# Kernel tuning notes

Hardware: AMD Instinct MI355X
Metric: run time of the kernel (lower is better)

## Reference

```python
import jax, jax.numpy as jnp
import numpy as np

B, SIDES, L = 8192, 2, 64   # batch, (left,right) trees, leaves per tree (complete binary tree)
V, D, C, R = 10000, 128, 128, 7  # vocab, word_dim, cpr_dim, num_rels


def setup_inputs() -> dict:
    key = jax.random.key(0)
    ks = jax.random.split(key, 9)
    s = 0.05
    return {
        "tokens": jax.random.randint(ks[0], (B, SIDES, L), 0, V, dtype=jnp.int32),
        "voc_w": jax.random.normal(ks[1], (V, D), dtype=jnp.float32) * s,
        "voc_b": jax.random.normal(ks[2], (D,), dtype=jnp.float32) * s,
        "cps_w": jax.random.normal(ks[3], (D, 2 * D), dtype=jnp.float32) * s,
        "cps_b": jax.random.normal(ks[4], (D,), dtype=jnp.float32) * s,
        "cpr_w": jax.random.normal(ks[5], (C, 2 * D), dtype=jnp.float32) * s,
        "cpr_b": jax.random.normal(ks[6], (C,), dtype=jnp.float32) * s,
        "sm_w": jax.random.normal(ks[7], (R, C), dtype=jnp.float32) * s,
        "sm_b": jax.random.normal(ks[8], (R,), dtype=jnp.float32) * s,
    }


def reference(tokens, voc_w, voc_b, cps_w, cps_b, cpr_w, cpr_b, sm_w, sm_b):
    # Leaf composition: one-hot @ Linear(voc_size, word_dim) == embedding gather + bias
    h = voc_w[tokens] + voc_b  # [B, 2, L, D]
    # Level-by-level composition of complete binary trees: cat(left,right) -> cps -> tanh
    n = h.shape[2]
    while n > 1:
        h = h.reshape(h.shape[0], SIDES, n // 2, 2 * h.shape[-1])  # adjacent pairs -> concat
        h = jnp.tanh(jnp.einsum('bsnk,dk->bsnd', h, cps_w) + cps_b)
        n //= 2
    root = h.reshape(h.shape[0], -1)  # [B, 2*D]: cat(left_cps, right_cps)
    z = jax.nn.leaky_relu(root @ cpr_w.T + cpr_b)  # LeakyReLU default slope 0.01
    return jax.nn.softmax(z @ sm_w.T + sm_b, axis=-1)  # [B, R]
```

## Files before the change

kernel.cpp:

```cpp
#include <hip/hip_runtime.h>
#include <hip/hip_bf16.h>


typedef __attribute__((ext_vector_type(8))) short bf16x8;
typedef __attribute__((ext_vector_type(4))) float f32x4;

#define VOCN (10000 * 128)
#define CPSN (128 * 256)
#define CPRN (128 * 256)

__device__ __forceinline__ uint pk2(float a, float b) {
  union { __hip_bfloat162 h2; uint u; } cv;
  cv.h2 = __float22bfloat162_rn(make_float2(a, b));
  return cv.u;
}
__device__ __forceinline__ float2 up2(uint u) {
  union { uint u; __hip_bfloat162 h2; } cv; cv.u = u;
  return __bfloat1622float2(cv.h2);
}
__device__ __forceinline__ float fast_tanh(float x) {
  const float t = x * x;
  float u = __builtin_fmaf(t, -0.05396825397f, 0.13333333333f);
  u = __builtin_fmaf(t, u, -0.33333333333f);
  u = __builtin_fmaf(t, u, 1.0f);
  return x * u;
}
__device__ __forceinline__ int sf(int r) { return r ^ ((r >> 3) & 7); }

__global__ void prep_kernel(const float* __restrict__ voc_w, const float* __restrict__ voc_b,
                            const float* __restrict__ cps_w, const float* __restrict__ cpr_w,
                            ushort* __restrict__ ws) {
  const int i4 = (blockIdx.x * 256 + threadIdx.x) * 4;
  if (i4 >= VOCN + CPSN + CPRN) return;
  float4 v;
  if (i4 < VOCN) {
    v = *(const float4*)(voc_w + i4);
    const float4 bb = *(const float4*)(voc_b + (i4 & 127));
    v.x += bb.x; v.y += bb.y; v.z += bb.z; v.w += bb.w;
  } else if (i4 < VOCN + CPSN) {
    v = *(const float4*)(cps_w + (i4 - VOCN));
  } else {
    v = *(const float4*)(cpr_w + (i4 - VOCN - CPSN));
  }
  uint2 w; w.x = pk2(v.x, v.y); w.y = pk2(v.z, v.w);
  *(uint2*)(ws + i4) = w;
}

#define MFMA16(Ax, Bx, Cx) __builtin_amdgcn_mfma_f32_16x16x32_bf16(Ax, Bx, Cx, 0, 0, 0)

template<int TOFF>
__device__ __forceinline__ void tile16(const char* hb, const bf16x8 (&A)[2][8],
                                       int RL, int RR, f32x4& aA, f32x4& aB) {
  bf16x8 bl[4], br[4];
#pragma unroll
  for (int q = 0; q < 4; ++q) {
    bl[q] = *(const bf16x8*)(hb + RL + TOFF + q * 4096);
    br[q] = *(const bf16x8*)(hb + RR + TOFF + q * 4096);
  }
#pragma unroll
  for (int q = 0; q < 4; ++q) {
    aA = MFMA16(A[0][q], bl[q], aA);
    aB = MFMA16(A[1][q], bl[q], aB);
  }
#pragma unroll
  for (int q = 0; q < 4; ++q) {
    aA = MFMA16(A[0][4 + q], br[q], aA);
    aB = MFMA16(A[1][4 + q], br[q], aB);
  }
}

template<int TOFF>
__device__ __forceinline__ void wtile(char* hb, int W, const f32x4& aA, const f32x4& aB) {
  uint2 w0, w1;
  w0.x = pk2(fast_tanh(aA[0]), fast_tanh(aA[1]));
  w0.y = pk2(fast_tanh(aA[2]), fast_tanh(aA[3]));
  w1.x = pk2(fast_tanh(aB[0]), fast_tanh(aB[1]));
  w1.y = pk2(fast_tanh(aB[2]), fast_tanh(aB[3]));
  *(uint2*)(hb + W + TOFF) = w0;
  *(uint2*)(hb + W + TOFF + 2048) = w1;
}

template<int PRE>
__global__ __launch_bounds__(256, 4)
void trnn_kernel(const int* __restrict__ tokens,
                 const float* __restrict__ voc_w, const float* __restrict__ voc_b,
                 const float* __restrict__ cps_w, const float* __restrict__ cps_b,
                 const float* __restrict__ cpr_w, const float* __restrict__ cpr_b,
                 const float* __restrict__ sm_w, const float* __restrict__ sm_b,
                 const ushort* __restrict__ wsb, float* __restrict__ out) {
  __shared__ ushort h[16384];
  const int tid = threadIdx.x;
  const int lane = tid & 63, wv = tid >> 6;
  const int l15 = lane & 15, lh = lane >> 4;
  const int b = blockIdx.x;
  char* hb = (char*)h;

  const ushort* voc_bf = wsb;
  const ushort* cps_bf = wsb + VOCN;
  const ushort* cpr_bf = wsb + VOCN + CPSN;

  const int lhb = lh * 1024;
  const int RLa = lhb + sf(2 * l15) * 16;
  const int RRa = lhb + sf(2 * l15 + 1) * 16;
  const int RLb = lhb + sf(2 * l15 + 32) * 16;
  const int RRb = lhb + sf(2 * l15 + 33) * 16;
  const int RL3 = (((l15 >> 3) & 1) << 14) + lhb + sf((l15 & 7) * 2) * 16;
  const int RR3 = (((l15 >> 3) & 1) << 14) + lhb + sf((l15 & 7) * 2 + 1) * 16;
  const int RL4 = (((l15 >> 2) & 1) << 14) + lhb + sf((l15 & 3) * 2) * 16;
  const int RR4 = (((l15 >> 2) & 1) << 14) + lhb + sf((l15 & 3) * 2 + 1) * 16;
  const int RL5 = (((l15 >> 1) & 1) << 14) + lhb + sf((l15 & 1) * 2) * 16;
  const int RR5 = (((l15 >> 1) & 1) << 14) + lhb + sf((l15 & 1) * 2 + 1) * 16;
  const int RL6 = ((l15 & 1) << 14) + lhb;
  const int RR6 = ((l15 & 1) << 14) + lhb + 16;
  const int dpart = (((wv * 32 + lh * 4) >> 3) << 10) + ((lh & 1) << 3);
  const int Wa = sf(l15) * 16 + dpart;
  const int Wb = sf(l15 + 16) * 16 + dpart;
  const int W3 = (((l15 >> 3) & 1) << 14) + sf(l15 & 7) * 16 + dpart;
  const int W4 = (((l15 >> 2) & 1) << 14) + sf(l15 & 3) * 16 + dpart;
  const int W5 = (((l15 >> 1) & 1) << 14) + sf(l15 & 1) * 16 + dpart;
  const int W6 = ((l15 & 1) << 14) + dpart;

  bf16x8 A[2][8];
  f32x4 bias[2];
#pragma unroll
  for (int mt = 0; mt < 2; ++mt) {
    const int d = wv * 32 + mt * 16 + l15;
#pragma unroll
    for (int kt = 0; kt < 8; ++kt) {
      const int k = kt * 32 + lh * 8;
      if constexpr (PRE) {
        A[mt][kt] = *(const bf16x8*)(cps_bf + d * 256 + k);
      } else {
        const float* p = cps_w + d * 256 + k;
        float4 lo = *(const float4*)p, hi = *(const float4*)(p + 4);
        union { bf16x8 v; uint4 u; } f;
        f.u.x = pk2(lo.x, lo.y); f.u.y = pk2(lo.z, lo.w);
        f.u.z = pk2(hi.x, hi.y); f.u.w = pk2(hi.z, hi.w);
        A[mt][kt] = f.v;
      }
    }
    const float4 bb = *(const float4*)(cps_b + wv * 32 + mt * 16 + lh * 4);
    bias[mt][0] = bb.x; bias[mt][1] = bb.y; bias[mt][2] = bb.z; bias[mt][3] = bb.w;
  }

  {
    const int tree = tid >> 7, lf = (tid >> 1) & 63, half = tid & 1;
    const int tok = tokens[b * 128 + tree * 64 + lf];
    char* tp = hb + tree * 16384 + half * 8192 + sf(lf) * 16;
    if constexpr (PRE) {
      const ushort* vr = voc_bf + tok * 128 + half * 64;
#pragma unroll
      for (int j = 0; j < 8; ++j)
        *(uint4*)(tp + j * 1024) = *(const uint4*)(vr + j * 8);
    } else {
      const float* vw = voc_w + tok * 128 + half * 64;
      const float* vb = voc_b + half * 64;
#pragma unroll
      for (int j = 0; j < 8; ++j) {
        float4 v0 = *(const float4*)(vw + j * 8);
        float4 v1 = *(const float4*)(vw + j * 8 + 4);
        float4 q0 = *(const float4*)(vb + j * 8);
        float4 q1 = *(const float4*)(vb + j * 8 + 4);
        uint4 w;
        w.x = pk2(v0.x + q0.x, v0.y + q0.y);
        w.y = pk2(v0.z + q0.z, v0.w + q0.w);
        w.z = pk2(v1.x + q1.x, v1.y + q1.y);
        w.w = pk2(v1.z + q1.z, v1.w + q1.w);
        *(uint4*)(tp + j * 1024) = w;
      }
    }
  }
  __syncthreads();

  {
    f32x4 a0 = bias[0], b0 = bias[1], a1 = bias[0], b1 = bias[1];
    f32x4 a2 = bias[0], b2 = bias[1], a3 = bias[0], b3 = bias[1];
    tile16<0>(hb, A, RLa, RRa, a0, b0);
    tile16<0>(hb, A, RLb, RRb, a1, b1);
    tile16<16384>(hb, A, RLa, RRa, a2, b2);
    tile16<16384>(hb, A, RLb, RRb, a3, b3);
    __syncthreads();
    wtile<0>(hb, Wa, a0, b0);
    wtile<0>(hb, Wb, a1, b1);
    wtile<16384>(hb, Wa, a2, b2);
    wtile<16384>(hb, Wb, a3, b3);
    __syncthreads();
  }
  {
    f32x4 a0 = bias[0], b0 = bias[1], a1 = bias[0], b1 = bias[1];
    tile16<0>(hb, A, RLa, RRa, a0, b0);
    tile16<16384>(hb, A, RLa, RRa, a1, b1);
    __syncthreads();
    wtile<0>(hb, Wa, a0, b0);
    wtile<16384>(hb, Wa, a1, b1);
    __syncthreads();
  }
  {
    f32x4 a0 = bias[0], b0 = bias[1];
    tile16<0>(hb, A, RL3, RR3, a0, b0);
    __syncthreads();
    wtile<0>(hb, W3, a0, b0);
    __syncthreads();
  }
  {
    f32x4 a0 = bias[0], b0 = bias[1];
    tile16<0>(hb, A, RL4, RR4, a0, b0);
    __syncthreads();
    if (l15 < 8) wtile<0>(hb, W4, a0, b0);
    __syncthreads();
  }
  {
    f32x4 a0 = bias[0], b0 = bias[1];
    tile16<0>(hb, A, RL5, RR5, a0, b0);
    __syncthreads();
    if (l15 < 4) wtile<0>(hb, W5, a0, b0);
    __syncthreads();
  }
  {
    f32x4 a0 = bias[0], b0 = bias[1];
    tile16<0>(hb, A, RL6, RR6, a0, b0);
    __syncthreads();
    if (l15 < 2) wtile<0>(hb, W6, a0, b0);
    __syncthreads();
  }


  {
    const int half = tid >> 7, c = tid & 127;
    const char* rp = hb + half * 16384;
    float acc = 0.f;
#pragma unroll 4
    for (int ch = 0; ch < 16; ++ch) {
      uint4 u = *(const uint4*)(rp + ch * 1024);
      float2 e0 = up2(u.x), e1 = up2(u.y), e2 = up2(u.z), e3 = up2(u.w);
      if constexpr (PRE) {
        uint4 wq = *(const uint4*)(cpr_bf + c * 256 + half * 128 + ch * 8);
        float2 w0 = up2(wq.x), w1 = up2(wq.y), w2 = up2(wq.z), w3 = up2(wq.w);
        acc += e0.x * w0.x + e0.y * w0.y + e1.x * w1.x + e1.y * w1.y
             + e2.x * w2.x + e2.y * w2.y + e3.x * w3.x + e3.y * w3.y;
      } else {
        const float* wr = cpr_w + c * 256 + half * 128 + ch * 8;
        float4 w0 = *(const float4*)wr, w1 = *(const float4*)(wr + 4);
        acc += e0.x * w0.x + e0.y * w0.y + e1.x * w0.z + e1.y * w0.w
             + e2.x * w1.x + e2.y * w1.y + e3.x * w1.z + e3.y * w1.w;
      }
    }
    *(float*)(hb + ((tid >> 4) << 10) + 512 + ((tid & 15) << 2)) = acc;
  }
  __syncthreads();
  if (tid < 128) {
    const float p0 = *(const float*)(hb + ((tid >> 4) << 10) + 512 + ((tid & 15) << 2));
    const int j1 = tid + 128;
    const float p1 = *(const float*)(hb + ((j1 >> 4) << 10) + 512 + ((j1 & 15) << 2));
    float z = p0 + p1 + cpr_b[tid];
    z = z > 0.f ? z : 0.01f * z;
    *(float*)(hb + 16384 + ((tid >> 3) << 10) + 768 + ((tid & 7) << 2)) = z;
  }
  __syncthreads();

  if (wv == 0) {
    const int i0 = lane, i1 = 64 + lane;
    const float za = *(const float*)(hb + 16384 + ((i0 >> 3) << 10) + 768 + ((i0 & 7) << 2));
    const float zc = *(const float*)(hb + 16384 + ((i1 >> 3) << 10) + 768 + ((i1 & 7) << 2));
    float p[7];
#pragma unroll
    for (int j = 0; j < 7; ++j)
      p[j] = za * sm_w[j * 128 + lane] + zc * sm_w[j * 128 + 64 + lane];
#pragma unroll
    for (int j = 0; j < 7; ++j) {
      float v = p[j];
#pragma unroll
      for (int off = 32; off >= 1; off >>= 1) v += __shfl_xor(v, off, 64);
      p[j] = v + sm_b[j];
    }
    float mx = p[0];
#pragma unroll
    for (int j = 1; j < 7; ++j) mx = fmaxf(mx, p[j]);
    float e[7], s = 0.f;
#pragma unroll
    for (int j = 0; j < 7; ++j) { e[j] = __expf(p[j] - mx); s += e[j]; }
    const float inv = 1.f / s;
    if (lane == 0) {
#pragma unroll
      for (int j = 0; j < 7; ++j) out[b * 7 + j] = e[j] * inv;
    }
  }
}

extern "C" void kernel_launch(void* const* d_in, const int* in_sizes, int n_in,
                              void* d_out, int out_size, void* d_ws, size_t ws_size,
                              hipStream_t stream) {
  const int*   tokens = (const int*)  d_in[0];
  const float* voc_w  = (const float*)d_in[1];
  const float* voc_b  = (const float*)d_in[2];
  const float* cps_w  = (const float*)d_in[3];
  const float* cps_b  = (const float*)d_in[4];
  const float* cpr_w  = (const float*)d_in[5];
  const float* cpr_b  = (const float*)d_in[6];
  const float* sm_w   = (const float*)d_in[7];
  const float* sm_b   = (const float*)d_in[8];
  float* out = (float*)d_out;

  const int B = in_sizes[0] / 128;
  const size_t need = (size_t)(VOCN + CPSN + CPRN) * sizeof(ushort);

  if (ws_size >= need) {
    ushort* ws = (ushort*)d_ws;
    const int tot4 = (VOCN + CPSN + CPRN) / 4;
    prep_kernel<<<(tot4 + 255) / 256, 256, 0, stream>>>(voc_w, voc_b, cps_w, cpr_w, ws);
    trnn_kernel<1><<<B, 256, 0, stream>>>(tokens, voc_w, voc_b, cps_w, cps_b,
                                          cpr_w, cpr_b, sm_w, sm_b, ws, out);
  } else {
    trnn_kernel<0><<<B, 256, 0, stream>>>(tokens, voc_w, voc_b, cps_w, cps_b,
                                          cpr_w, cpr_b, sm_w, sm_b,
                                          (const ushort*)d_ws, out);
  }
}
```

Baseline: 166.8 us.

## Use 512-thread blocks with one wave group per tree side

Doubles the block to 512 threads. Waves 4-7 handle the right tree and waves 0-3 the left, so each wave does half the MFMA tiles per level. The leaf gather and the cpr reduction are split four ways, and the partial sums are combined in shared memory. The aim is more waves in flight to hide LDS and MFMA latency. In exchange, every wave now loads its own copy of the cps A-fragments into registers, and occupancy limits from the register budget may change under launch_bounds(512,4).

```diff
diff --git a/kernel.cpp b/kernel.cpp
--- a/kernel.cpp
+++ b/kernel.cpp
@@ -48,14 +48,13 @@
 
 #define MFMA16(Ax, Bx, Cx) __builtin_amdgcn_mfma_f32_16x16x32_bf16(Ax, Bx, Cx, 0, 0, 0)
 
-template<int TOFF>
 __device__ __forceinline__ void tile16(const char* hb, const bf16x8 (&A)[2][8],
                                        int RL, int RR, f32x4& aA, f32x4& aB) {
   bf16x8 bl[4], br[4];
 #pragma unroll
   for (int q = 0; q < 4; ++q) {
-    bl[q] = *(const bf16x8*)(hb + RL + TOFF + q * 4096);
-    br[q] = *(const bf16x8*)(hb + RR + TOFF + q * 4096);
+    bl[q] = *(const bf16x8*)(hb + RL + q * 4096);
+    br[q] = *(const bf16x8*)(hb + RR + q * 4096);
   }
 #pragma unroll
   for (int q = 0; q < 4; ++q) {
@@ -69,19 +68,18 @@
   }
 }
 
-template<int TOFF>
 __device__ __forceinline__ void wtile(char* hb, int W, const f32x4& aA, const f32x4& aB) {
   uint2 w0, w1;
   w0.x = pk2(fast_tanh(aA[0]), fast_tanh(aA[1]));
   w0.y = pk2(fast_tanh(aA[2]), fast_tanh(aA[3]));
   w1.x = pk2(fast_tanh(aB[0]), fast_tanh(aB[1]));
   w1.y = pk2(fast_tanh(aB[2]), fast_tanh(aB[3]));
-  *(uint2*)(hb + W + TOFF) = w0;
-  *(uint2*)(hb + W + TOFF + 2048) = w1;
+  *(uint2*)(hb + W) = w0;
+  *(uint2*)(hb + W + 2048) = w1;
 }
 
 template<int PRE>
-__global__ __launch_bounds__(256, 4)
+__global__ __launch_bounds__(512, 4)
 void trnn_kernel(const int* __restrict__ tokens,
                  const float* __restrict__ voc_w, const float* __restrict__ voc_b,
                  const float* __restrict__ cps_w, const float* __restrict__ cps_b,
@@ -92,6 +90,8 @@
   const int tid = threadIdx.x;
   const int lane = tid & 63, wv = tid >> 6;
   const int l15 = lane & 15, lh = lane >> 4;
+  const int wq = wv & 3;
+  const int toff = (wv >> 2) << 14;
   const int b = blockIdx.x;
   char* hb = (char*)h;
 
@@ -99,32 +99,32 @@
   const ushort* cps_bf = wsb + VOCN;
   const ushort* cpr_bf = wsb + VOCN + CPSN;
 
-  const int lhb = lh * 1024;
+  const int lhb = toff + lh * 1024;
   const int RLa = lhb + sf(2 * l15) * 16;
   const int RRa = lhb + sf(2 * l15 + 1) * 16;
   const int RLb = lhb + sf(2 * l15 + 32) * 16;
   const int RRb = lhb + sf(2 * l15 + 33) * 16;
-  const int RL3 = (((l15 >> 3) & 1) << 14) + lhb + sf((l15 & 7) * 2) * 16;
-  const int RR3 = (((l15 >> 3) & 1) << 14) + lhb + sf((l15 & 7) * 2 + 1) * 16;
-  const int RL4 = (((l15 >> 2) & 1) << 14) + lhb + sf((l15 & 3) * 2) * 16;
-  const int RR4 = (((l15 >> 2) & 1) << 14) + lhb + sf((l15 & 3) * 2 + 1) * 16;
-  const int RL5 = (((l15 >> 1) & 1) << 14) + lhb + sf((l15 & 1) * 2) * 16;
-  const int RR5 = (((l15 >> 1) & 1) << 14) + lhb + sf((l15 & 1) * 2 + 1) * 16;
-  const int RL6 = ((l15 & 1) << 14) + lhb;
-  const int RR6 = ((l15 & 1) << 14) + lhb + 16;
-  const int dpart = (((wv * 32 + lh * 4) >> 3) << 10) + ((lh & 1) << 3);
+  const int RL3 = lhb + sf((l15 & 7) * 2) * 16;
+  const int RR3 = lhb + sf((l15 & 7) * 2 + 1) * 16;
+  const int RL4 = lhb + sf((l15 & 3) * 2) * 16;
+  const int RR4 = lhb + sf((l15 & 3) * 2 + 1) * 16;
+  const int RL5 = lhb + sf((l15 & 1) * 2) * 16;
+  const int RR5 = lhb + sf((l15 & 1) * 2 + 1) * 16;
+  const int RL6 = lhb;
+  const int RR6 = lhb + 16;
+  const int dpart = toff + (((wq * 32 + lh * 4) >> 3) << 10) + ((lh & 1) << 3);
   const int Wa = sf(l15) * 16 + dpart;
   const int Wb = sf(l15 + 16) * 16 + dpart;
-  const int W3 = (((l15 >> 3) & 1) << 14) + sf(l15 & 7) * 16 + dpart;
-  const int W4 = (((l15 >> 2) & 1) << 14) + sf(l15 & 3) * 16 + dpart;
-  const int W5 = (((l15 >> 1) & 1) << 14) + sf(l15 & 1) * 16 + dpart;
-  const int W6 = ((l15 & 1) << 14) + dpart;
+  const int W3 = sf(l15 & 7) * 16 + dpart;
+  const int W4 = sf(l15 & 3) * 16 + dpart;
+  const int W5 = sf(l15 & 1) * 16 + dpart;
+  const int W6 = dpart;
 
   bf16x8 A[2][8];
   f32x4 bias[2];
 #pragma unroll
   for (int mt = 0; mt < 2; ++mt) {
-    const int d = wv * 32 + mt * 16 + l15;
+    const int d = wq * 32 + mt * 16 + l15;
 #pragma unroll
     for (int kt = 0; kt < 8; ++kt) {
       const int k = kt * 32 + lh * 8;
@@ -139,24 +139,24 @@
         A[mt][kt] = f.v;
       }
     }
-    const float4 bb = *(const float4*)(cps_b + wv * 32 + mt * 16 + lh * 4);
+    const float4 bb = *(const float4*)(cps_b + wq * 32 + mt * 16 + lh * 4);
     bias[mt][0] = bb.x; bias[mt][1] = bb.y; bias[mt][2] = bb.z; bias[mt][3] = bb.w;
   }
 
   {
-    const int tree = tid >> 7, lf = (tid >> 1) & 63, half = tid & 1;
+    const int tree = tid >> 8, lf = (tid >> 2) & 63, qr = tid & 3;
     const int tok = tokens[b * 128 + tree * 64 + lf];
-    char* tp = hb + tree * 16384 + half * 8192 + sf(lf) * 16;
+    char* tp = hb + tree * 16384 + qr * 4096 + sf(lf) * 16;
     if constexpr (PRE) {
-      const ushort* vr = voc_bf + tok * 128 + half * 64;
-#pragma unroll
-      for (int j = 0; j < 8; ++j)
+      const ushort* vr = voc_bf + tok * 128 + qr * 32;
+#pragma unroll
+      for (int j = 0; j < 4; ++j)
         *(uint4*)(tp + j * 1024) = *(const uint4*)(vr + j * 8);
     } else {
-      const float* vw = voc_w + tok * 128 + half * 64;
-      const float* vb = voc_b + half * 64;
-#pragma unroll
-      for (int j = 0; j < 8; ++j) {
+      const float* vw = voc_w + tok * 128 + qr * 32;
+      const float* vb = voc_b + qr * 32;
+#pragma unroll
+      for (int j = 0; j < 4; ++j) {
         float4 v0 = *(const float4*)(vw + j * 8);
         float4 v1 = *(const float4*)(vw + j * 8 + 4);
         float4 q0 = *(const float4*)(vb + j * 8);
@@ -174,85 +174,77 @@
 
   {
     f32x4 a0 = bias[0], b0 = bias[1], a1 = bias[0], b1 = bias[1];
-    f32x4 a2 = bias[0], b2 = bias[1], a3 = bias[0], b3 = bias[1];
-    tile16<0>(hb, A, RLa, RRa, a0, b0);
-    tile16<0>(hb, A, RLb, RRb, a1, b1);
-    tile16<16384>(hb, A, RLa, RRa, a2, b2);
-    tile16<16384>(hb, A, RLb, RRb, a3, b3);
-    __syncthreads();
-    wtile<0>(hb, Wa, a0, b0);
-    wtile<0>(hb, Wb, a1, b1);
-    wtile<16384>(hb, Wa, a2, b2);
-    wtile<16384>(hb, Wb, a3, b3);
-    __syncthreads();
-  }
-  {
-    f32x4 a0 = bias[0], b0 = bias[1], a1 = bias[0], b1 = bias[1];
-    tile16<0>(hb, A, RLa, RRa, a0, b0);
-    tile16<16384>(hb, A, RLa, RRa, a1, b1);
-    __syncthreads();
-    wtile<0>(hb, Wa, a0, b0);
-    wtile<16384>(hb, Wa, a1, b1);
-    __syncthreads();
-  }
-  {
-    f32x4 a0 = bias[0], b0 = bias[1];
-    tile16<0>(hb, A, RL3, RR3, a0, b0);
-    __syncthreads();
-    wtile<0>(hb, W3, a0, b0);
-    __syncthreads();
-  }
-  {
-    f32x4 a0 = bias[0], b0 = bias[1];
-    tile16<0>(hb, A, RL4, RR4, a0, b0);
-    __syncthreads();
-    if (l15 < 8) wtile<0>(hb, W4, a0, b0);
-    __syncthreads();
-  }
-  {
-    f32x4 a0 = bias[0], b0 = bias[1];
-    tile16<0>(hb, A, RL5, RR5, a0, b0);
-    __syncthreads();
-    if (l15 < 4) wtile<0>(hb, W5, a0, b0);
-    __syncthreads();
-  }
-  {
-    f32x4 a0 = bias[0], b0 = bias[1];
-    tile16<0>(hb, A, RL6, RR6, a0, b0);
-    __syncthreads();
-    if (l15 < 2) wtile<0>(hb, W6, a0, b0);
-    __syncthreads();
-  }
-
-
-  {
-    const int half = tid >> 7, c = tid & 127;
-    const char* rp = hb + half * 16384;
+    tile16(hb, A, RLa, RRa, a0, b0);
+    tile16(hb, A, RLb, RRb, a1, b1);
+    __syncthreads();
+    wtile(hb, Wa, a0, b0);
+    wtile(hb, Wb, a1, b1);
+    __syncthreads();
+  }
+  {
+    f32x4 a0 = bias[0], b0 = bias[1];
+    tile16(hb, A, RLa, RRa, a0, b0);
+    __syncthreads();
+    wtile(hb, Wa, a0, b0);
+    __syncthreads();
+  }
+  {
+    f32x4 a0 = bias[0], b0 = bias[1];
+    tile16(hb, A, RL3, RR3, a0, b0);
+    __syncthreads();
+    if (l15 < 8) wtile(hb, W3, a0, b0);
+    __syncthreads();
+  }
+  {
+    f32x4 a0 = bias[0], b0 = bias[1];
+    tile16(hb, A, RL4, RR4, a0, b0);
+    __syncthreads();
+    if (l15 < 4) wtile(hb, W4, a0, b0);
+    __syncthreads();
+  }
+  {
+    f32x4 a0 = bias[0], b0 = bias[1];
+    tile16(hb, A, RL5, RR5, a0, b0);
+    __syncthreads();
+    if (l15 < 2) wtile(hb, W5, a0, b0);
+    __syncthreads();
+  }
+  {
+    f32x4 a0 = bias[0], b0 = bias[1];
+    tile16(hb, A, RL6, RR6, a0, b0);
+    __syncthreads();
+    if (l15 == 0) wtile(hb, W6, a0, b0);
+    __syncthreads();
+  }
+
+
+  {
+    const int q = tid >> 7, c = tid & 127;
+    const char* rp = hb + (q >> 1) * 16384 + (q & 1) * 8192;
     float acc = 0.f;
 #pragma unroll 4
-    for (int ch = 0; ch < 16; ++ch) {
-      uint4 u = *(const uint4*)(rp + ch * 1024);
+    for (int j = 0; j < 8; ++j) {
+      uint4 u = *(const uint4*)(rp + j * 1024);
       float2 e0 = up2(u.x), e1 = up2(u.y), e2 = up2(u.z), e3 = up2(u.w);
       if constexpr (PRE) {
-        uint4 wq = *(const uint4*)(cpr_bf + c * 256 + half * 128 + ch * 8);
-        float2 w0 = up2(wq.x), w1 = up2(wq.y), w2 = up2(wq.z), w3 = up2(wq.w);
+        uint4 wqd = *(const uint4*)(cpr_bf + c * 256 + (q >> 1) * 128 + ((q & 1) * 8 + j) * 8);
+        float2 w0 = up2(wqd.x), w1 = up2(wqd.y), w2 = up2(wqd.z), w3 = up2(wqd.w);
         acc += e0.x * w0.x + e0.y * w0.y + e1.x * w1.x + e1.y * w1.y
              + e2.x * w2.x + e2.y * w2.y + e3.x * w3.x + e3.y * w3.y;
       } else {
-        const float* wr = cpr_w + c * 256 + half * 128 + ch * 8;
+        const float* wr = cpr_w + c * 256 + (q >> 1) * 128 + ((q & 1) * 8 + j) * 8;
         float4 w0 = *(const float4*)wr, w1 = *(const float4*)(wr + 4);
         acc += e0.x * w0.x + e0.y * w0.y + e1.x * w0.z + e1.y * w0.w
              + e2.x * w1.x + e2.y * w1.y + e3.x * w1.z + e3.y * w1.w;
       }
     }
-    *(float*)(hb + ((tid >> 4) << 10) + 512 + ((tid & 15) << 2)) = acc;
+    *(float*)(hb + ((c >> 3) << 10) + 512 + ((c & 7) << 2) + (q << 5)) = acc;
   }
   __syncthreads();
   if (tid < 128) {
-    const float p0 = *(const float*)(hb + ((tid >> 4) << 10) + 512 + ((tid & 15) << 2));
-    const int j1 = tid + 128;
-    const float p1 = *(const float*)(hb + ((j1 >> 4) << 10) + 512 + ((j1 & 15) << 2));
-    float z = p0 + p1 + cpr_b[tid];
+    const int cb = ((tid >> 3) << 10) + 512 + ((tid & 7) << 2);
+    float z = *(const float*)(hb + cb) + *(const float*)(hb + cb + 32)
+            + *(const float*)(hb + cb + 64) + *(const float*)(hb + cb + 96) + cpr_b[tid];
     z = z > 0.f ? z : 0.01f * z;
     *(float*)(hb + 16384 + ((tid >> 3) << 10) + 768 + ((tid & 7) << 2)) = z;
   }
@@ -308,10 +300,10 @@
     ushort* ws = (ushort*)d_ws;
     const int tot4 = (VOCN + CPSN + CPRN) / 4;
     prep_kernel<<<(tot4 + 255) / 256, 256, 0, stream>>>(voc_w, voc_b, cps_w, cpr_w, ws);
-    trnn_kernel<1><<<B, 256, 0, stream>>>(tokens, voc_w, voc_b, cps_w, cps_b,
+    trnn_kernel<1><<<B, 512, 0, stream>>>(tokens, voc_w, voc_b, cps_w, cps_b,
                                           cpr_w, cpr_b, sm_w, sm_b, ws, out);
   } else {
-    trnn_kernel<0><<<B, 256, 0, stream>>>(tokens, voc_w, voc_b, cps_w, cps_b,
+    trnn_kernel<0><<<B, 512, 0, stream>>>(tokens, voc_w, voc_b, cps_w, cps_b,
                                           cpr_w, cpr_b, sm_w, sm_b,
                                           (const ushort*)d_ws, out);
   }
```

New measurement: 245.2 us. +47.0%, slower.
